# Optimization experiments

Hardware: AMD Instinct MI355X
Metric: run time of the kernel (lower is better)

The kernel has to match this reference:

```python
import jax, jax.numpy as jnp
import numpy as np

N, N_BINS = 100000, 512
BATCH, K = 8192, 16


def setup_inputs() -> dict:
    key = jax.random.key(0)
    k1, k2, k3 = jax.random.split(key, 3)
    outputs = jax.random.uniform(k1, (N, N_BINS), dtype=jnp.float32)
    # y holds (float-encoded) neighbor indices; trunc(y) must index rows of outputs
    y = jax.random.randint(k2, (BATCH, K), 0, N).astype(jnp.float32)
    weights = jax.random.uniform(k3, (BATCH,), dtype=jnp.float32)
    return {"outputs": outputs, "y": y, "weights": weights}


def reference(outputs, y, weights):
    n, n_bins = outputs.shape
    batch_size, k = y.shape
    nns = jnp.trunc(y).astype(jnp.int32)  # (B, k) indices into outputs rows

    # Torch builds add[a,b,c] = outputs[nns[c,a], b] + outputs[c, b] with shape
    # (k, n_bins, batch) then maxes over bins. Equivalent, batch-major layout:
    o_nn = outputs[nns]  # (B, k, n_bins) gather
    add = jnp.max(o_nn + outputs[:batch_size, None, :], axis=-1)  # (B, k)

    booster_weights = jnp.clip((2.0 - jnp.mean(add, axis=1)) / 2.0, 0.5)  # (B,)
    add_mean = jnp.mean(add * weights[:, None])
    diff = jnp.square(2.0 - add_mean)

    target_b = n / n_bins
    b_col = jnp.sum(outputs[:batch_size], axis=0)  # (n_bins,)
    b = jnp.max(b_col) - jnp.min(b_col)

    cost = b / target_b + diff
    return (cost, diff, b / target_b, booster_weights)
```

## Files before the change

kernel.cpp:

```cpp
#include <hip/hip_runtime.h>

#define NBINS 512

__global__ void init_ws_kernel(float* __restrict__ ws, int n) {
    int t = blockIdx.x * blockDim.x + threadIdx.x;
    if (t < n) ws[t] = 0.0f;
}

__global__ __launch_bounds__(1024) void main_kernel(
        const float* __restrict__ outputs,
        const float* __restrict__ y,
        const float* __restrict__ weights,
        float* __restrict__ out,
        float* __restrict__ accum,
        int K) {
    __shared__ float4 sbase[NBINS / 4];
    __shared__ float s_add[16];

    const int b = blockIdx.x;
    const int t = threadIdx.x;

    if (t < NBINS / 4)
        sbase[t] = ((const float4*)(outputs + (size_t)b * NBINS))[t];
    __syncthreads();

    const int w = t >> 6;
    const int lane = t & 63;

    const int nn = (int)y[b * K + w];
    const float4* rp = (const float4*)(outputs + (size_t)nn * NBINS);
    float4 g0 = rp[lane * 2];
    float4 g1 = rp[lane * 2 + 1];
    float4 b0 = sbase[lane * 2];
    float4 b1 = sbase[lane * 2 + 1];

    float m = fmaxf(fmaxf(fmaxf(g0.x + b0.x, g0.y + b0.y),
                          fmaxf(g0.z + b0.z, g0.w + b0.w)),
                    fmaxf(fmaxf(g1.x + b1.x, g1.y + b1.y),
                          fmaxf(g1.z + b1.z, g1.w + b1.w)));

    #pragma unroll
    for (int off = 32; off > 0; off >>= 1)
        m = fmaxf(m, __shfl_down(m, off, 64));

    if (lane == 0) s_add[w] = m;
    __syncthreads();

    if (t == 0) {
        float sum = 0.0f;
        #pragma unroll
        for (int i = 0; i < 16; ++i) sum += s_add[i];
        float mean = sum * (1.0f / 16.0f);
        float booster = fmaxf(0.5f, (2.0f - mean) * 0.5f);
        out[3 + b] = booster;
        atomicAdd(&accum[b & 255], weights[b] * sum);
    }
}

__global__ void colsum_kernel(const float* __restrict__ outputs,
                              float* __restrict__ bcol,
                              int rows_per_block) {
    const int t = threadIdx.x;
    const int r0 = blockIdx.x * rows_per_block;
    float local = 0.0f;
    for (int r = 0; r < rows_per_block; ++r)
        local += outputs[(size_t)(r0 + r) * NBINS + t];
    atomicAdd(&bcol[t], local);
}

__global__ void final_kernel(const float* __restrict__ bcol,
                             const float* __restrict__ accum,
                             float* __restrict__ out,
                             float inv_count, float inv_target) {
    __shared__ float smax[NBINS];
    __shared__ float smin[NBINS];
    const int t = threadIdx.x;
    float v = bcol[t];
    smax[t] = v;
    smin[t] = v;
    __syncthreads();
    for (int s = NBINS / 2; s > 0; s >>= 1) {
        if (t < s) {
            smax[t] = fmaxf(smax[t], smax[t + s]);
            smin[t] = fminf(smin[t], smin[t + s]);
        }
        __syncthreads();
    }
    if (t == 0) {
        float acc = 0.0f;
        for (int i = 0; i < 256; ++i) acc += accum[i];
        float add_mean = acc * inv_count;
        float d = 2.0f - add_mean;
        float diff = d * d;
        float bn = (smax[0] - smin[0]) * inv_target;
        out[0] = bn + diff;
        out[1] = diff;
        out[2] = bn;
    }
}

extern "C" void kernel_launch(void* const* d_in, const int* in_sizes, int n_in,
                              void* d_out, int out_size, void* d_ws, size_t ws_size,
                              hipStream_t stream) {
    const float* outputs = (const float*)d_in[0];
    const float* y       = (const float*)d_in[1];
    const float* weights = (const float*)d_in[2];
    float* out = (float*)d_out;

    const int B = in_sizes[2];
    const int K = in_sizes[1] / B;
    const int N = in_sizes[0] / NBINS;

    float* ws    = (float*)d_ws;
    float* bcol  = ws;
    float* accum = ws + NBINS;

    init_ws_kernel<<<1, 1024, 0, stream>>>(ws, NBINS + 256);

    main_kernel<<<B, K * 64, 0, stream>>>(outputs, y, weights, out, accum, K);

    const int rows_per_block = 128;
    colsum_kernel<<<B / rows_per_block, NBINS, 0, stream>>>(outputs, bcol, rows_per_block);

    final_kernel<<<1, NBINS, 0, stream>>>(bcol, accum, out,
                                          1.0f / (float)(B * K),
                                          (float)NBINS / (float)N);
}
```

Measured before the change: 326.2 us.

## Split gather into per-wave multi-neighbor kernel, replace atomics with partial buffers

```diff
diff --git a/kernel.cpp b/kernel.cpp
--- a/kernel.cpp
+++ b/kernel.cpp
@@ -1,81 +1,109 @@
 #include <hip/hip_runtime.h>
 
 #define NBINS 512
+#define BDIM 256
 
-__global__ void init_ws_kernel(float* __restrict__ ws, int n) {
-    int t = blockIdx.x * blockDim.x + threadIdx.x;
-    if (t < n) ws[t] = 0.0f;
-}
-
-__global__ __launch_bounds__(1024) void main_kernel(
+__global__ __launch_bounds__(BDIM) void gather_kernel(
         const float* __restrict__ outputs,
         const float* __restrict__ y,
-        const float* __restrict__ weights,
-        float* __restrict__ out,
-        float* __restrict__ accum,
+        float* __restrict__ add,
         int K) {
-    __shared__ float4 sbase[NBINS / 4];
-    __shared__ float s_add[16];
+    const int b    = blockIdx.x;
+    const int w    = threadIdx.x >> 6;
+    const int lane = threadIdx.x & 63;
 
-    const int b = blockIdx.x;
-    const int t = threadIdx.x;
+    const float4* bp = (const float4*)(outputs + (size_t)b * NBINS);
+    const float4  b0 = bp[lane * 2];
+    const float4  b1 = bp[lane * 2 + 1];
 
-    if (t < NBINS / 4)
-        sbase[t] = ((const float4*)(outputs + (size_t)b * NBINS))[t];
-    __syncthreads();
+    const int kbase = w * 4;
+    int nn[4];
+    #pragma unroll
+    for (int j = 0; j < 4; ++j)
+        nn[j] = (int)y[b * K + kbase + j];
 
-    const int w = t >> 6;
-    const int lane = t & 63;
+    float4 g0[4], g1[4];
+    #pragma unroll
+    for (int j = 0; j < 4; ++j) {
+        const float4* gp = (const float4*)(outputs + (size_t)nn[j] * NBINS);
+        g0[j] = gp[lane * 2];
+        g1[j] = gp[lane * 2 + 1];
+    }
 
-    const int nn = (int)y[b * K + w];
-    const float4* rp = (const float4*)(outputs + (size_t)nn * NBINS);
-    float4 g0 = rp[lane * 2];
-    float4 g1 = rp[lane * 2 + 1];
-    float4 b0 = sbase[lane * 2];
-    float4 b1 = sbase[lane * 2 + 1];
-
-    float m = fmaxf(fmaxf(fmaxf(g0.x + b0.x, g0.y + b0.y),
-                          fmaxf(g0.z + b0.z, g0.w + b0.w)),
-                    fmaxf(fmaxf(g1.x + b1.x, g1.y + b1.y),
-                          fmaxf(g1.z + b1.z, g1.w + b1.w)));
+    float m[4];
+    #pragma unroll
+    for (int j = 0; j < 4; ++j) {
+        m[j] = fmaxf(fmaxf(fmaxf(g0[j].x + b0.x, g0[j].y + b0.y),
+                           fmaxf(g0[j].z + b0.z, g0[j].w + b0.w)),
+                     fmaxf(fmaxf(g1[j].x + b1.x, g1[j].y + b1.y),
+                           fmaxf(g1[j].z + b1.z, g1[j].w + b1.w)));
+    }
 
     #pragma unroll
-    for (int off = 32; off > 0; off >>= 1)
-        m = fmaxf(m, __shfl_down(m, off, 64));
+    for (int off = 32; off > 0; off >>= 1) {
+        #pragma unroll
+        for (int j = 0; j < 4; ++j)
+            m[j] = fmaxf(m[j], __shfl_down(m[j], off, 64));
+    }
 
-    if (lane == 0) s_add[w] = m;
-    __syncthreads();
-
-    if (t == 0) {
-        float sum = 0.0f;
-        #pragma unroll
-        for (int i = 0; i < 16; ++i) sum += s_add[i];
-        float mean = sum * (1.0f / 16.0f);
-        float booster = fmaxf(0.5f, (2.0f - mean) * 0.5f);
-        out[3 + b] = booster;
-        atomicAdd(&accum[b & 255], weights[b] * sum);
+    if (lane == 0) {
+        float4 v = make_float4(m[0], m[1], m[2], m[3]);
+        *((float4*)(add + (size_t)b * K + kbase)) = v;
     }
 }
 
-__global__ void colsum_kernel(const float* __restrict__ outputs,
-                              float* __restrict__ bcol,
-                              int rows_per_block) {
+__global__ __launch_bounds__(NBINS) void colsum_kernel(
+        const float* __restrict__ outputs,
+        float* __restrict__ part,
+        int rows_per_block) {
     const int t = threadIdx.x;
-    const int r0 = blockIdx.x * rows_per_block;
+    const size_t r0 = (size_t)blockIdx.x * rows_per_block;
     float local = 0.0f;
     for (int r = 0; r < rows_per_block; ++r)
-        local += outputs[(size_t)(r0 + r) * NBINS + t];
-    atomicAdd(&bcol[t], local);
+        local += outputs[(r0 + r) * NBINS + t];
+    part[(size_t)blockIdx.x * NBINS + t] = local;
 }
 
-__global__ void final_kernel(const float* __restrict__ bcol,
-                             const float* __restrict__ accum,
-                             float* __restrict__ out,
-                             float inv_count, float inv_target) {
+__global__ __launch_bounds__(BDIM) void booster_kernel(
+        const float* __restrict__ add,
+        const float* __restrict__ weights,
+        float* __restrict__ out,
+        float* __restrict__ wpartial,
+        int K) {
+    __shared__ float sred[BDIM];
+    const int t = threadIdx.x;
+    const int b = blockIdx.x * BDIM + t;
+
+    const float4* ap = (const float4*)(add + (size_t)b * K);
+    float4 a0 = ap[0], a1 = ap[1], a2 = ap[2], a3 = ap[3];
+    float sum = ((a0.x + a0.y) + (a0.z + a0.w))
+              + ((a1.x + a1.y) + (a1.z + a1.w))
+              + ((a2.x + a2.y) + (a2.z + a2.w))
+              + ((a3.x + a3.y) + (a3.z + a3.w));
+
+    float booster = fmaxf(0.5f, (2.0f - sum * (1.0f / 16.0f)) * 0.5f);
+    out[3 + b] = booster;
+
+    sred[t] = weights[b] * sum;
+    __syncthreads();
+    for (int s = BDIM / 2; s > 0; s >>= 1) {
+        if (t < s) sred[t] += sred[t + s];
+        __syncthreads();
+    }
+    if (t == 0) wpartial[blockIdx.x] = sred[0];
+}
+
+__global__ __launch_bounds__(NBINS) void final_kernel(
+        const float* __restrict__ part,
+        const float* __restrict__ wpartial,
+        float* __restrict__ out,
+        int npart, int nw, float inv_count, float inv_target) {
     __shared__ float smax[NBINS];
     __shared__ float smin[NBINS];
     const int t = threadIdx.x;
-    float v = bcol[t];
+    float v = 0.0f;
+    for (int j = 0; j < npart; ++j)
+        v += part[(size_t)j * NBINS + t];
     smax[t] = v;
     smin[t] = v;
     __syncthreads();
@@ -88,7 +116,7 @@
     }
     if (t == 0) {
         float acc = 0.0f;
-        for (int i = 0; i < 256; ++i) acc += accum[i];
+        for (int i = 0; i < nw; ++i) acc += wpartial[i];
         float add_mean = acc * inv_count;
         float d = 2.0f - add_mean;
         float diff = d * d;
@@ -111,18 +139,20 @@
     const int K = in_sizes[1] / B;
     const int N = in_sizes[0] / NBINS;
 
-    float* ws    = (float*)d_ws;
-    float* bcol  = ws;
-    float* accum = ws + NBINS;
+    const int COL_BLOCKS = 256;
+    const int rows_per_block = B / COL_BLOCKS;
+    const int BOOST_BLOCKS = B / BDIM;
 
-    init_ws_kernel<<<1, 1024, 0, stream>>>(ws, NBINS + 256);
+    float* ws      = (float*)d_ws;
+    float* add     = ws;
+    float* colpart = add + (size_t)B * K;
+    float* wpart   = colpart + (size_t)COL_BLOCKS * NBINS;
 
-    main_kernel<<<B, K * 64, 0, stream>>>(outputs, y, weights, out, accum, K);
-
-    const int rows_per_block = 128;
-    colsum_kernel<<<B / rows_per_block, NBINS, 0, stream>>>(outputs, bcol, rows_per_block);
-
-    final_kernel<<<1, NBINS, 0, stream>>>(bcol, accum, out,
+    gather_kernel<<<B, BDIM, 0, stream>>>(outputs, y, add, K);
+    colsum_kernel<<<COL_BLOCKS, NBINS, 0, stream>>>(outputs, colpart, rows_per_block);
+    booster_kernel<<<BOOST_BLOCKS, BDIM, 0, stream>>>(add, weights, out, wpart, K);
+    final_kernel<<<1, NBINS, 0, stream>>>(colpart, wpart, out,
+                                          COL_BLOCKS, BOOST_BLOCKS,
                                           1.0f / (float)(B * K),
                                           (float)NBINS / (float)N);
 }
```

Result: slower. 350.1 us (+7.3%).
